# Optimization experiments

Measured on AMD Instinct MI355X. Metric: run time of the kernel, lower is better.

The kernel has to match this reference:

```python
import jax, jax.numpy as jnp
import numpy as np

EPS = 1e-6
D_CONV = 4

def _layernorm(x):
    m = jnp.mean(x, axis=-1, keepdims=True)
    v = jnp.mean((x - m) ** 2, axis=-1, keepdims=True)
    return (x - m) / jnp.sqrt(v + EPS)

def setup_inputs() -> dict:
    key = jax.random.key(0)
    ks = jax.random.split(key, 20)
    B, L, D = 2, 4096, 1024
    Di = D          # expand = 1
    N = 16          # d_state
    R = 64          # dt_rank = ceil(D/16)
    H = 4 * D       # mlp hidden
    s = 0.02
    rn = lambda k, sh: s * jax.random.normal(k, sh, dtype=jnp.float32)
    x = jax.random.normal(ks[0], (B, L, D), dtype=jnp.float32)
    path = jax.random.permutation(ks[1], L).astype(jnp.int32)
    path_rev = jnp.argsort(path).astype(jnp.int32)
    A_log = jnp.log(jnp.tile(jnp.arange(1, N + 1, dtype=jnp.float32)[None, :], (Di, 1)))
    return {
        'x': x, 'path': path, 'path_rev': path_rev,
        'in_proj_w': rn(ks[2], (2 * Di, D)),
        'conv_w': rn(ks[3], (Di, D_CONV)), 'conv_b': rn(ks[4], (Di,)),
        'x_proj_w': rn(ks[5], (R + 2 * N, Di)),
        'dt_proj_w': rn(ks[6], (Di, R)), 'dt_proj_b': rn(ks[7], (Di,)),
        'A_log': A_log, 'D_param': jnp.ones((Di,), dtype=jnp.float32),
        'out_proj_w': rn(ks[8], (D, Di)),
        'fc1_w': rn(ks[9], (H, D)), 'fc1_b': jnp.zeros((H,), dtype=jnp.float32),
        'fc2_w': rn(ks[10], (D, H)), 'fc2_b': jnp.zeros((D,), dtype=jnp.float32),
    }

def _mamba(u, in_proj_w, conv_w, conv_b, x_proj_w, dt_proj_w, dt_proj_b, A_log, D_param, out_proj_w):
    B, L, _ = u.shape
    N = A_log.shape[1]
    R = dt_proj_w.shape[1]
    xz = u @ in_proj_w.T                      # (B,L,2*Di)
    xi, z = jnp.split(xz, 2, axis=-1)
    # causal depthwise conv1d, kernel 4
    xpad = jnp.pad(xi, ((0, 0), (D_CONV - 1, 0), (0, 0)))
    xc = conv_b + sum(conv_w[:, k] * xpad[:, k:k + L, :] for k in range(D_CONV))
    xc = jax.nn.silu(xc)                      # (B,L,Di)
    proj = xc @ x_proj_w.T                    # (B,L,R+2N)
    dt_r = proj[..., :R]
    Bm = proj[..., R:R + N]                   # (B,L,N)
    Cm = proj[..., R + N:]                    # (B,L,N)
    dt = jax.nn.softplus(dt_r @ dt_proj_w.T + dt_proj_b)  # (B,L,Di)
    A = -jnp.exp(A_log)                       # (Di,N)

    def step(h, inp):
        dt_t, B_t, C_t, x_t = inp             # (B,Di),(B,N),(B,N),(B,Di)
        dA = jnp.exp(dt_t[:, :, None] * A)    # (B,Di,N)
        h = dA * h + (dt_t * x_t)[:, :, None] * B_t[:, None, :]
        y = jnp.einsum('bdn,bn->bd', h, C_t)
        return h, y

    h0 = jnp.zeros((B, xc.shape[-1], N), dtype=u.dtype)
    xs = (dt.transpose(1, 0, 2), Bm.transpose(1, 0, 2), Cm.transpose(1, 0, 2), xc.transpose(1, 0, 2))
    _, ys = jax.lax.scan(step, h0, xs)        # (L,B,Di)
    y = ys.transpose(1, 0, 2) + D_param * xc
    y = y * jax.nn.silu(z)
    return y @ out_proj_w.T

def reference(x, path, path_rev, in_proj_w, conv_w, conv_b, x_proj_w, dt_proj_w, dt_proj_b,
              A_log, D_param, out_proj_w, fc1_w, fc1_b, fc2_w, fc2_b):
    tmp1 = x[:, path, :]                      # zigzag gather
    tmp1 = _mamba(_layernorm(tmp1), in_proj_w, conv_w, conv_b, x_proj_w,
                  dt_proj_w, dt_proj_b, A_log, D_param, out_proj_w)
    x = x + tmp1[:, path_rev, :]              # zigzag scatter (inverse gather)
    h = _layernorm(x)
    h = jax.nn.gelu(h @ fc1_w.T + fc1_b, approximate=True) @ fc2_w.T + fc2_b
    return x + h
```

## Files before the change

kernel.cpp:

```cpp
#include <hip/hip_runtime.h>
#include <cstdint>
#include <cstddef>

typedef unsigned short u16;
typedef __bf16 bf16x8 __attribute__((ext_vector_type(8)));
typedef float f32x4 __attribute__((ext_vector_type(4)));
typedef u16 u16x8 __attribute__((ext_vector_type(8)));

#define B_ 2
#define L_ 4096
#define D_ 1024
#define N_ 16
#define BL_ 8192
#define NC_ 64
#define LC_ 64

__device__ __forceinline__ float bf2f(u16 h) {
  union { unsigned int u; float f; } v; v.u = ((unsigned int)h) << 16; return v.f;
}
__device__ __forceinline__ u16 f2bf(float f) {
  union { float f; unsigned int u; } v; v.f = f;
  unsigned int r = v.u + 0x7FFFu + ((v.u >> 16) & 1u);
  return (u16)(r >> 16);
}
__device__ __forceinline__ float sigmoidf_(float x) { return 1.0f / (1.0f + __expf(-x)); }

#define WBF_TOT 11730944
__global__ __launch_bounds__(256) void cvt_w_k(
    const float* __restrict__ s0, const float* __restrict__ s1,
    const float* __restrict__ s2, const float* __restrict__ s3,
    const float* __restrict__ s4, const float* __restrict__ s5,
    u16* __restrict__ dst)
{
  int i = blockIdx.x * 256 + threadIdx.x;
  if (i >= WBF_TOT) return;
  float v;
  if (i < 2097152) v = s0[i];
  else if (i < 2228224) { int j = i - 2097152; v = (j < 98304) ? s1[j] : 0.0f; }
  else if (i < 2293760) v = s2[i - 2228224];
  else if (i < 3342336) v = s3[i - 2293760];
  else if (i < 7536640) v = s4[i - 3342336];
  else v = s5[i - 7536640];
  dst[i] = f2bf(v);
}

#define BK 32
enum { M_BF16 = 0, M_PROJ = 1, M_SOFTPLUS = 2, M_GELU = 3, M_BIASRES = 4 };

#define GLDS(gp, lp) __builtin_amdgcn_global_load_lds( \
    (const __attribute__((address_space(1))) void*)(gp), \
    (__attribute__((address_space(3))) void*)(lp), 16, 0, 0)

template<int MODE>
__device__ __forceinline__ void epi_store(
    float v, size_t row, int col, int Nn,
    float* __restrict__ C, u16* __restrict__ C2,
    const float* __restrict__ bias, const u16* __restrict__ resid)
{
  if constexpr (MODE == M_BF16) {
    C2[row * Nn + col] = f2bf(v);
  } else if constexpr (MODE == M_PROJ) {
    C[row * 96 + col] = v;
    if (col < 64) C2[(row << 6) + col] = f2bf(v);
  } else if constexpr (MODE == M_SOFTPLUS) {
    v += bias[col];
    v = (v > 20.0f) ? v : log1pf(__expf(v));
    C2[row * Nn + col] = f2bf(v);
  } else if constexpr (MODE == M_GELU) {
    v += bias[col];
    float a = 0.7978845608028654f * (v + 0.044715f * v * v * v);
    float t = 1.0f - 2.0f / (__expf(2.0f * a) + 1.0f);
    C2[row * Nn + col] = f2bf(0.5f * v * (1.0f + t));
  } else if constexpr (MODE == M_BIASRES) {
    C[row * Nn + col] = v + bias[col] + bf2f(resid[row * Nn + col]);
  }
}

#define BM 128
#define BN 128

template<int MODE, int K>
__global__ __launch_bounds__(256, 2) void gemm_bt(
    const u16* __restrict__ A, const u16* __restrict__ W,
    float* __restrict__ C, u16* __restrict__ C2,
    const float* __restrict__ bias, const u16* __restrict__ resid,
    int M, int N)
{
  __shared__ __align__(16) u16 As[3][BM * BK];
  __shared__ __align__(16) u16 Bs[3][BN * BK];

  const int id = blockIdx.x + gridDim.x * blockIdx.y;
  const int xcd = id & 7;
  const int qq = id >> 3;
  const int bandH = gridDim.y >> 3;
  const int xs = qq % gridDim.x;
  const int ys = xcd * bandH + qq / gridDim.x;
  const int bm = ys * BM;
  const int bn = xs * BN;

  const int tid = threadIdx.x;
  const int lane = tid & 63;
  const int wave = tid >> 6;
  const int wr = (wave >> 1) * 64;
  const int wc = (wave & 1) * 64;

  f32x4 acc[4][4];
#pragma unroll
  for (int i = 0; i < 4; ++i)
#pragma unroll
    for (int j = 0; j < 4; ++j)
#pragma unroll
      for (int r = 0; r < 4; ++r) acc[i][j][r] = 0.0f;

  const int r0 = tid >> 2;
  const int ke = (((tid & 3) ^ (r0 & 3)) << 3);
  const u16* Ab = A + (size_t)(bm + r0) * K + ke;
  const u16* Wb = W + (size_t)(bn + r0) * K + ke;
  constexpr size_t rstep = (size_t)64 * K;

  auto issue = [&](int buf, int k0) {
    GLDS(Ab + k0, &As[buf][tid * 8]);
    GLDS(Ab + k0 + rstep, &As[buf][(tid + 256) * 8]);
    GLDS(Wb + k0, &Bs[buf][tid * 8]);
    GLDS(Wb + k0 + rstep, &Bs[buf][(tid + 256) * 8]);
  };

  issue(0, 0);
  if constexpr (BK < K) issue(1, BK);

  const int mr = lane & 15;
  const int pos = (((lane >> 4) ^ (mr & 3)) << 3);
  constexpr int NIT = K / BK;

  auto step = [&](int it) {
    if (it + 1 < NIT) asm volatile("s_waitcnt vmcnt(4)" ::: "memory");
    else              asm volatile("s_waitcnt vmcnt(0)" ::: "memory");
    asm volatile("s_barrier" ::: "memory");
    if (it + 2 < NIT) issue((it + 2) % 3, (it + 2) * BK);
    const int cur = it % 3;
    bf16x8 af[4], bfr[4];
#pragma unroll
    for (int i = 0; i < 4; ++i)
      af[i] = *(const bf16x8*)(&As[cur][(wr + i * 16 + mr) * BK + pos]);
#pragma unroll
    for (int j = 0; j < 4; ++j)
      bfr[j] = *(const bf16x8*)(&Bs[cur][(wc + j * 16 + mr) * BK + pos]);
#pragma unroll
    for (int i = 0; i < 4; ++i)
#pragma unroll
      for (int j = 0; j < 4; ++j)
        acc[i][j] = __builtin_amdgcn_mfma_f32_16x16x32_bf16(af[i], bfr[j], acc[i][j], 0, 0, 0);
  };

  if constexpr (NIT <= 32) {
#pragma unroll
    for (int it = 0; it < NIT; ++it) step(it);
  } else {
#pragma unroll 6
    for (int it = 0; it < NIT; ++it) step(it);
  }

  const int mlo = (lane >> 4) << 2;
  const int nlo = lane & 15;
#pragma unroll
  for (int i = 0; i < 4; ++i) {
#pragma unroll
    for (int j = 0; j < 4; ++j) {
      int col = bn + wc + j * 16 + nlo;
      if (col < N) {
#pragma unroll
        for (int r = 0; r < 4; ++r) {
          size_t row = (size_t)(bm + wr + i * 16 + mlo + r);
          epi_store<MODE>(acc[i][j][r], row, col, N, C, C2, bias, resid);
        }
      }
    }
  }
}

#define BM2 128
#define BN2 256

template<int MODE, int K>
__global__ __launch_bounds__(256, 2) void gemm_big(
    const u16* __restrict__ A, const u16* __restrict__ W,
    float* __restrict__ C, u16* __restrict__ C2,
    const float* __restrict__ bias, const u16* __restrict__ resid,
    int M, int N)
{
  __shared__ __align__(16) u16 As[3][BM2 * BK];
  __shared__ __align__(16) u16 Bs[3][BN2 * BK];

  const int id = blockIdx.x + gridDim.x * blockIdx.y;
  const int xcd = id & 7;
  const int qq = id >> 3;
  const int bandH = gridDim.y >> 3;
  const int xs = qq % gridDim.x;
  const int ys = xcd * bandH + qq / gridDim.x;
  const int bm = ys * BM2;
  const int bn = xs * BN2;

  const int tid = threadIdx.x;
  const int lane = tid & 63;
  const int wave = tid >> 6;
  const int wm = (wave >> 1) * 64;
  const int wn = (wave & 1) * 128;

  f32x4 acc[4][8];
#pragma unroll
  for (int i = 0; i < 4; ++i)
#pragma unroll
    for (int j = 0; j < 8; ++j)
#pragma unroll
      for (int r = 0; r < 4; ++r) acc[i][j][r] = 0.0f;

  const int r0 = tid >> 2;
  const int ke = (((tid & 3) ^ (r0 & 3)) << 3);
  const u16* Ab = A + (size_t)(bm + r0) * K + ke;
  const u16* Wb = W + (size_t)(bn + r0) * K + ke;
  constexpr size_t rstep = (size_t)64 * K;

  auto issue = [&](int buf, int k0) {
    GLDS(Ab + k0, &As[buf][tid * 8]);
    GLDS(Ab + k0 + rstep, &As[buf][(tid + 256) * 8]);
    GLDS(Wb + k0, &Bs[buf][tid * 8]);
    GLDS(Wb + k0 + rstep,     &Bs[buf][(tid + 256) * 8]);
    GLDS(Wb + k0 + 2 * rstep, &Bs[buf][(tid + 512) * 8]);
    GLDS(Wb + k0 + 3 * rstep, &Bs[buf][(tid + 768) * 8]);
  };

  issue(0, 0);
  issue(1, BK);

  const int mr = lane & 15;
  const int pos = (((lane >> 4) ^ (mr & 3)) << 3);
  constexpr int NIT = K / BK;

  auto step = [&](int it) {
    if (it + 1 < NIT) asm volatile("s_waitcnt vmcnt(6)" ::: "memory");
    else              asm volatile("s_waitcnt vmcnt(0)" ::: "memory");
    asm volatile("s_barrier" ::: "memory");
    if (it + 2 < NIT) issue((it + 2) % 3, (it + 2) * BK);
    const int cur = it % 3;
    bf16x8 af[4], bfr[8];
#pragma unroll
    for (int i = 0; i < 4; ++i)
      af[i] = *(const bf16x8*)(&As[cur][(wm + i * 16 + mr) * BK + pos]);
#pragma unroll
    for (int j = 0; j < 8; ++j)
      bfr[j] = *(const bf16x8*)(&Bs[cur][(wn + j * 16 + mr) * BK + pos]);
#pragma unroll
    for (int i = 0; i < 4; ++i)
#pragma unroll
      for (int j = 0; j < 8; ++j)
        acc[i][j] = __builtin_amdgcn_mfma_f32_16x16x32_bf16(af[i], bfr[j], acc[i][j], 0, 0, 0);
  };

  if constexpr (NIT <= 32) {
#pragma unroll
    for (int it = 0; it < NIT; ++it) step(it);
  } else {
#pragma unroll 6
    for (int it = 0; it < NIT; ++it) step(it);
  }

  const int mlo = (lane >> 4) << 2;
  const int nlo = lane & 15;
#pragma unroll
  for (int i = 0; i < 4; ++i) {
#pragma unroll
    for (int j = 0; j < 8; ++j) {
      int col = bn + wn + j * 16 + nlo;
#pragma unroll
      for (int r = 0; r < 4; ++r) {
        size_t row = (size_t)(bm + wm + i * 16 + mlo + r);
        epi_store<MODE>(acc[i][j][r], row, col, N, C, C2, bias, resid);
      }
    }
  }
}

__device__ __forceinline__ void blockReduce2(float& s, float& q) {
#pragma unroll
  for (int o = 32; o > 0; o >>= 1) { s += __shfl_down(s, o, 64); q += __shfl_down(q, o, 64); }
  __shared__ float red[2][4];
  int lane = threadIdx.x & 63, wave = threadIdx.x >> 6;
  if (lane == 0) { red[0][wave] = s; red[1][wave] = q; }
  __syncthreads();
  s = red[0][0] + red[0][1] + red[0][2] + red[0][3];
  q = red[1][0] + red[1][1] + red[1][2] + red[1][3];
}

__global__ __launch_bounds__(256) void ln_gather_k(
    const float* __restrict__ x, const int* __restrict__ path, u16* __restrict__ out)
{
  int b = blockIdx.x >> 12;
  int l = blockIdx.x & 4095;
  int src = path[l];
  const float* row = x + (((size_t)b * L_ + src) << 10);
  u16* orow = out + (((size_t)b * L_ + l) << 10);
  float v[4], s = 0.f, q = 0.f;
#pragma unroll
  for (int i = 0; i < 4; ++i) {
    v[i] = row[threadIdx.x + (i << 8)];
    s += v[i]; q += v[i] * v[i];
  }
  blockReduce2(s, q);
  float mean = s * (1.0f / 1024.0f);
  float var = q * (1.0f / 1024.0f) - mean * mean;
  float rstd = rsqrtf(var + 1e-6f);
#pragma unroll
  for (int i = 0; i < 4; ++i)
    orow[threadIdx.x + (i << 8)] = f2bf((v[i] - mean) * rstd);
}

__global__ __launch_bounds__(256) void ln_scatter_k(
    const float* __restrict__ x, const int* __restrict__ prev,
    const u16* __restrict__ mo, u16* __restrict__ xnew, u16* __restrict__ lnout)
{
  int b = blockIdx.x >> 12;
  int l = blockIdx.x & 4095;
  int pl = prev[l];
  const float* xr = x + (((size_t)b * L_ + l) << 10);
  const u16* mr_ = mo + (((size_t)b * L_ + pl) << 10);
  size_t base = ((size_t)blockIdx.x) << 10;
  float v[4], s = 0.f, q = 0.f;
#pragma unroll
  for (int i = 0; i < 4; ++i) {
    v[i] = xr[threadIdx.x + (i << 8)] + bf2f(mr_[threadIdx.x + (i << 8)]);
    s += v[i]; q += v[i] * v[i];
  }
  blockReduce2(s, q);
  float mean = s * (1.0f / 1024.0f);
  float var = q * (1.0f / 1024.0f) - mean * mean;
  float rstd = rsqrtf(var + 1e-6f);
#pragma unroll
  for (int i = 0; i < 4; ++i) {
    xnew[base + threadIdx.x + (i << 8)] = f2bf(v[i]);
    lnout[base + threadIdx.x + (i << 8)] = f2bf((v[i] - mean) * rstd);
  }
}

__global__ __launch_bounds__(256) void conv_silu_k(
    const u16* __restrict__ xz, const float* __restrict__ cw, const float* __restrict__ cb,
    u16* __restrict__ xc)
{
  int t = blockIdx.x * 256 + threadIdx.x;
  int d0 = (t & 127) << 3;
  int l  = (t >> 7) & 4095;
  int b  = t >> 19;
  float acc[8];
  f32x4 cb0 = *(const f32x4*)(&cb[d0]);
  f32x4 cb1 = *(const f32x4*)(&cb[d0 + 4]);
#pragma unroll
  for (int j = 0; j < 4; ++j) { acc[j] = cb0[j]; acc[4 + j] = cb1[j]; }
  f32x4 cwv[8];
#pragma unroll
  for (int j = 0; j < 8; ++j) cwv[j] = *(const f32x4*)(&cw[(d0 + j) << 2]);
#pragma unroll
  for (int k = 0; k < 4; ++k) {
    int ls = l + k - 3;
    if (ls >= 0) {
      u16x8 v = *(const u16x8*)(&xz[(((size_t)b * L_ + ls) << 11) + d0]);
#pragma unroll
      for (int j = 0; j < 8; ++j)
        acc[j] += cwv[j][k] * bf2f(v[j]);
    }
  }
  u16x8 o;
#pragma unroll
  for (int j = 0; j < 8; ++j) {
    float a = acc[j];
    a = a * sigmoidf_(a);
    o[j] = f2bf(a);
  }
  *(u16x8*)(&xc[(size_t)t << 3]) = o;
}

__global__ __launch_bounds__(256) void scan_p1_k(
    const u16* __restrict__ dt, const u16* __restrict__ xc, const float* __restrict__ proj,
    const float* __restrict__ A_log, float* __restrict__ acum, float* __restrict__ hloc)
{
  int c = blockIdx.x & (NC_ - 1);
  int q = (blockIdx.x >> 6) & 3;
  int b = blockIdx.x >> 8;
  int d = (q << 8) + threadIdx.x;
  float Arow[N_];
#pragma unroll
  for (int n = 0; n < N_; ++n) Arow[n] = -__expf(A_log[(d << 4) + n]);
  float h[N_], ac[N_];
#pragma unroll
  for (int n = 0; n < N_; ++n) { h[n] = 0.0f; ac[n] = 1.0f; }
  int l0 = c << 6;
  for (int i = 0; i < LC_; ++i) {
    size_t rowb = (size_t)b * L_ + (l0 + i);
    float dtv = bf2f(dt[(rowb << 10) + d]);
    float xv = bf2f(xc[(rowb << 10) + d]);
    float dtx = dtv * xv;
    const float* Bp = proj + rowb * 96 + 64;
#pragma unroll
    for (int n = 0; n < N_; ++n) {
      float dA = __expf(dtv * Arow[n]);
      h[n] = dA * h[n] + dtx * Bp[n];
      ac[n] *= dA;
    }
  }
  size_t sb = ((((size_t)b << 10) + d) << 10) + (c << 4);
#pragma unroll
  for (int n = 0; n < N_; ++n) { acum[sb + n] = ac[n]; hloc[sb + n] = h[n]; }
}

__global__ __launch_bounds__(256) void scan_p2_k(
    const float* __restrict__ acum, const float* __restrict__ hloc, float* __restrict__ hin)
{
  int idx = blockIdx.x * 256 + threadIdx.x;
  int n = idx & 15;
  int dn = idx >> 4;
  size_t base = ((size_t)dn << 10) + n;
  float hs = 0.0f;
  for (int c = 0; c < NC_; ++c) {
    hin[base + (c << 4)] = hs;
    hs = acum[base + (c << 4)] * hs + hloc[base + (c << 4)];
  }
}

__global__ __launch_bounds__(256) void scan_p3_k(
    const u16* __restrict__ dt, const u16* __restrict__ xc, const float* __restrict__ proj,
    const float* __restrict__ A_log, const float* __restrict__ Dp, const float* __restrict__ hin,
    const u16* __restrict__ xz, u16* __restrict__ yg)
{
  int c = blockIdx.x & (NC_ - 1);
  int q = (blockIdx.x >> 6) & 3;
  int b = blockIdx.x >> 8;
  int d = (q << 8) + threadIdx.x;
  float Arow[N_];
#pragma unroll
  for (int n = 0; n < N_; ++n) Arow[n] = -__expf(A_log[(d << 4) + n]);
  float h[N_];
  size_t sb = ((((size_t)b << 10) + d) << 10) + (c << 4);
#pragma unroll
  for (int n = 0; n < N_; ++n) h[n] = hin[sb + n];
  float Dv = Dp[d];
  int l0 = c << 6;
  for (int i = 0; i < LC_; ++i) {
    size_t rowb = (size_t)b * L_ + (l0 + i);
    float dtv = bf2f(dt[(rowb << 10) + d]);
    float xv = bf2f(xc[(rowb << 10) + d]);
    float dtx = dtv * xv;
    const float* Bp = proj + rowb * 96 + 64;
    const float* Cp = proj + rowb * 96 + 80;
    float y = 0.0f;
#pragma unroll
    for (int n = 0; n < N_; ++n) {
      float dA = __expf(dtv * Arow[n]);
      h[n] = dA * h[n] + dtx * Bp[n];
      y += h[n] * Cp[n];
    }
    y += Dv * xv;
    float zv = bf2f(xz[(rowb << 11) + 1024 + d]);
    yg[(rowb << 10) + d] = f2bf(y * zv * sigmoidf_(zv));
  }
}

extern "C" void kernel_launch(void* const* d_in, const int* in_sizes, int n_in,
                              void* d_out, int out_size, void* d_ws, size_t ws_size,
                              hipStream_t stream)
{
  const float* x_in      = (const float*)d_in[0];
  const int*   path      = (const int*)d_in[1];
  const int*   path_rev  = (const int*)d_in[2];
  const float* in_proj_w = (const float*)d_in[3];
  const float* conv_w    = (const float*)d_in[4];
  const float* conv_b    = (const float*)d_in[5];
  const float* x_proj_w  = (const float*)d_in[6];
  const float* dt_proj_w = (const float*)d_in[7];
  const float* dt_proj_b = (const float*)d_in[8];
  const float* A_log     = (const float*)d_in[9];
  const float* Dp        = (const float*)d_in[10];
  const float* out_pw    = (const float*)d_in[11];
  const float* fc1_w     = (const float*)d_in[12];
  const float* fc1_b     = (const float*)d_in[13];
  const float* fc2_w     = (const float*)d_in[14];
  const float* fc2_b     = (const float*)d_in[15];
  float* out = (float*)d_out;

  char* w = (char*)d_ws;
  size_t off = 0;
  auto alloc = [&](size_t bytes) -> char* {
    char* p = w + off;
    off = (off + bytes + 255) & ~(size_t)255;
    return p;
  };
  u16*   wbf   = (u16*)  alloc((size_t)WBF_TOT * 2);
  u16*   ln_bf = (u16*)  alloc((size_t)BL_ * 1024 * 2);
  u16*   xz    = (u16*)  alloc((size_t)BL_ * 2048 * 2);
  u16*   xc    = (u16*)  alloc((size_t)BL_ * 1024 * 2);
  char*  pool0 = alloc(0);
  float* proj  = (float*)alloc((size_t)BL_ * 96 * 4);
  u16*   dtr   = (u16*)  alloc((size_t)BL_ * 64 * 2);
  u16*   dt    = (u16*)  alloc((size_t)BL_ * 1024 * 2);
  float* acum  = (float*)alloc((size_t)2 * 1024 * NC_ * 16 * 4);
  float* hloc  = (float*)alloc((size_t)2 * 1024 * NC_ * 16 * 4);
  float* hin   = (float*)alloc((size_t)2 * 1024 * NC_ * 16 * 4);
  u16*   yg    = (u16*)  alloc((size_t)BL_ * 1024 * 2);
  u16*   h1b   = (u16*)pool0;
  off = (size_t)(pool0 - w) + ((size_t)BL_ * 4096 * 2);
  u16*   xnew  = (u16*)  alloc((size_t)BL_ * 1024 * 2);
  u16*   mo    = xz;

  const u16* w_inp = wbf;
  const u16* w_xp  = wbf + 2097152;
  const u16* w_dtp = wbf + 2228224;
  const u16* w_op  = wbf + 2293760;
  const u16* w_fc1 = wbf + 3342336;
  const u16* w_fc2 = wbf + 7536640;

  dim3 blk(256);
  cvt_w_k<<<WBF_TOT / 256, blk, 0, stream>>>(in_proj_w, x_proj_w, dt_proj_w, out_pw,
                                             fc1_w, fc2_w, wbf);
  ln_gather_k<<<BL_, blk, 0, stream>>>(x_in, path, ln_bf);
  gemm_big<M_BF16, 1024><<<dim3(8, 64), blk, 0, stream>>>(ln_bf, w_inp, nullptr, xz, nullptr, nullptr, 8192, 2048);
  conv_silu_k<<<(BL_ * 128) / 256, blk, 0, stream>>>(xz, conv_w, conv_b, xc);
  gemm_bt<M_PROJ, 1024><<<dim3(1, 64), blk, 0, stream>>>(xc, w_xp, proj, dtr, nullptr, nullptr, 8192, 96);
  gemm_bt<M_SOFTPLUS, 64><<<dim3(8, 64), blk, 0, stream>>>(dtr, w_dtp, nullptr, dt, dt_proj_b, nullptr, 8192, 1024);
  scan_p1_k<<<2 * 4 * NC_, blk, 0, stream>>>(dt, xc, proj, A_log, acum, hloc);
  scan_p2_k<<<(2 * 1024 * 16) / 256, blk, 0, stream>>>(acum, hloc, hin);
  scan_p3_k<<<2 * 4 * NC_, blk, 0, stream>>>(dt, xc, proj, A_log, Dp, hin, xz, yg);
  gemm_bt<M_BF16, 1024><<<dim3(8, 64), blk, 0, stream>>>(yg, w_op, nullptr, mo, nullptr, nullptr, 8192, 1024);
  ln_scatter_k<<<BL_, blk, 0, stream>>>(x_in, path_rev, mo, xnew, ln_bf);
  gemm_big<M_GELU, 1024><<<dim3(16, 64), blk, 0, stream>>>(ln_bf, w_fc1, nullptr, h1b, fc1_b, nullptr, 8192, 4096);
  gemm_bt<M_BIASRES, 4096><<<dim3(8, 64), blk, 0, stream>>>(h1b, w_fc2, out, nullptr, fc2_b, xnew, 8192, 1024);
}
```

Measured before the change: 583.0 us.

## Use 256x256 eight-phase pipelined GEMM and split-K fc2 with combine kernel

Replaces the 128x256 GEMM with a 512-thread kernel using 256x256 tiles and 64-wide K steps. It double-buffers LDS and interleaves LDS reads, global-to-LDS staging and MFMA work across eight phases, with s_setprio raised around the MFMA blocks. The in_proj and fc1 GEMMs move to this kernel. fc2 is also split along K into two fp32 partial buffers that reuse the dead ln_bf/xz/xc region, and a new elementwise kernel adds the partials, bias and residual. The larger tiles aim to raise operand reuse per LDS byte and hide memory latency. The cost is heavier register/LDS use and extra fp32 partial-sum traffic for fc2.

```diff
diff --git a/kernel.cpp b/kernel.cpp
--- a/kernel.cpp
+++ b/kernel.cpp
@@ -45,7 +45,7 @@
 }
 
 #define BK 32
-enum { M_BF16 = 0, M_PROJ = 1, M_SOFTPLUS = 2, M_GELU = 3, M_BIASRES = 4 };
+enum { M_BF16 = 0, M_PROJ = 1, M_SOFTPLUS = 2, M_GELU = 3, M_BIASRES = 4, M_F32 = 5 };
 
 #define GLDS(gp, lp) __builtin_amdgcn_global_load_lds( \
     (const __attribute__((address_space(1))) void*)(gp), \
@@ -73,6 +73,8 @@
     C2[row * Nn + col] = f2bf(0.5f * v * (1.0f + t));
   } else if constexpr (MODE == M_BIASRES) {
     C[row * Nn + col] = v + bias[col] + bf2f(resid[row * Nn + col]);
+  } else if constexpr (MODE == M_F32) {
+    C[row * Nn + col] = v;
   }
 }
 
@@ -178,18 +180,27 @@
   }
 }
 
-#define BM2 128
-#define BN2 256
-
-template<int MODE, int K>
-__global__ __launch_bounds__(256, 2) void gemm_big(
+#define P_MID asm volatile("s_barrier" ::: "memory")
+#define P_END asm volatile("s_barrier" ::: "memory")
+#define P_LG0 asm volatile("s_waitcnt lgkmcnt(0)" ::: "memory")
+#define P_VM2 asm volatile("s_waitcnt vmcnt(2)" ::: "memory")
+#define P_SB0 __builtin_amdgcn_sched_barrier(0)
+
+#define PH(RD1, RD2, STG, MH, NH, VMW) \
+  RD1; RD2; STG; \
+  P_MID; P_LG0; P_SB0; \
+  __builtin_amdgcn_s_setprio(1); mm(MH, NH); P_SB0; __builtin_amdgcn_s_setprio(0); \
+  VMW; P_END;
+
+template<int MODE, int KFULL, int KSPLIT>
+__global__ __launch_bounds__(512, 2) void gemm256(
     const u16* __restrict__ A, const u16* __restrict__ W,
     float* __restrict__ C, u16* __restrict__ C2,
     const float* __restrict__ bias, const u16* __restrict__ resid,
     int M, int N)
 {
-  __shared__ __align__(16) u16 As[3][BM2 * BK];
-  __shared__ __align__(16) u16 Bs[3][BN2 * BK];
+  __shared__ __align__(16) u16 As[2][16384];
+  __shared__ __align__(16) u16 Bs[2][16384];
 
   const int id = blockIdx.x + gridDim.x * blockIdx.y;
   const int xcd = id & 7;
@@ -197,87 +208,122 @@
   const int bandH = gridDim.y >> 3;
   const int xs = qq % gridDim.x;
   const int ys = xcd * bandH + qq / gridDim.x;
-  const int bm = ys * BM2;
-  const int bn = xs * BN2;
+  const int bm = ys * 256;
+  const int bn = xs * 256;
+  const int z = blockIdx.z;
 
   const int tid = threadIdx.x;
   const int lane = tid & 63;
   const int wave = tid >> 6;
-  const int wm = (wave >> 1) * 64;
-  const int wn = (wave & 1) * 128;
-
-  f32x4 acc[4][8];
-#pragma unroll
-  for (int i = 0; i < 4; ++i)
-#pragma unroll
-    for (int j = 0; j < 8; ++j)
+  const int wm = (wave >> 2) * 128;
+  const int wn = (wave & 3) * 64;
+  const int mr = lane & 15;
+  const int kq = lane >> 4;
+
+  f32x4 acc[8][4];
+#pragma unroll
+  for (int i = 0; i < 8; ++i)
+#pragma unroll
+    for (int j = 0; j < 4; ++j)
 #pragma unroll
       for (int r = 0; r < 4; ++r) acc[i][j][r] = 0.0f;
 
-  const int r0 = tid >> 2;
-  const int ke = (((tid & 3) ^ (r0 & 3)) << 3);
-  const u16* Ab = A + (size_t)(bm + r0) * K + ke;
-  const u16* Wb = W + (size_t)(bn + r0) * K + ke;
-  constexpr size_t rstep = (size_t)64 * K;
-
-  auto issue = [&](int buf, int k0) {
-    GLDS(Ab + k0, &As[buf][tid * 8]);
-    GLDS(Ab + k0 + rstep, &As[buf][(tid + 256) * 8]);
-    GLDS(Wb + k0, &Bs[buf][tid * 8]);
-    GLDS(Wb + k0 + rstep,     &Bs[buf][(tid + 256) * 8]);
-    GLDS(Wb + k0 + 2 * rstep, &Bs[buf][(tid + 512) * 8]);
-    GLDS(Wb + k0 + 3 * rstep, &Bs[buf][(tid + 768) * 8]);
-  };
-
-  issue(0, 0);
-  issue(1, BK);
-
-  const int mr = lane & 15;
-  const int pos = (((lane >> 4) ^ (mr & 3)) << 3);
-  constexpr int NIT = K / BK;
-
-  auto step = [&](int it) {
-    if (it + 1 < NIT) asm volatile("s_waitcnt vmcnt(6)" ::: "memory");
-    else              asm volatile("s_waitcnt vmcnt(0)" ::: "memory");
-    asm volatile("s_barrier" ::: "memory");
-    if (it + 2 < NIT) issue((it + 2) % 3, (it + 2) * BK);
-    const int cur = it % 3;
-    bf16x8 af[4], bfr[8];
-#pragma unroll
-    for (int i = 0; i < 4; ++i)
-      af[i] = *(const bf16x8*)(&As[cur][(wm + i * 16 + mr) * BK + pos]);
-#pragma unroll
-    for (int j = 0; j < 8; ++j)
-      bfr[j] = *(const bf16x8*)(&Bs[cur][(wn + j * 16 + mr) * BK + pos]);
-#pragma unroll
-    for (int i = 0; i < 4; ++i)
-#pragma unroll
-      for (int j = 0; j < 8; ++j)
-        acc[i][j] = __builtin_amdgcn_mfma_f32_16x16x32_bf16(af[i], bfr[j], acc[i][j], 0, 0, 0);
-  };
-
-  if constexpr (NIT <= 32) {
-#pragma unroll
-    for (int it = 0; it < NIT; ++it) step(it);
-  } else {
-#pragma unroll 6
-    for (int it = 0; it < NIT; ++it) step(it);
-  }
+  const int row0 = tid >> 3;
+  const int g = (tid & 7) ^ (row0 & 7);
+  const u16* Asrc = A + (size_t)(bm + row0) * KFULL + (size_t)z * KSPLIT + g * 8;
+  const u16* Wsrc = W + (size_t)(bn + row0) * KFULL + (size_t)z * KSPLIT + g * 8;
+
+  auto stage = [&](int buf, int which , int T) {
+    const int h = which & 1;
+    const u16* s = ((which < 2) ? Asrc : Wsrc) + (size_t)(h * 128) * KFULL + T * 64;
+    u16* d = (which < 2) ? &As[buf][h * 8192] : &Bs[buf][h * 8192];
+    GLDS(s, d + tid * 8);
+    GLDS(s + (size_t)64 * KFULL, d + (tid + 512) * 8);
+  };
+
+  bf16x8 Ar[8], Br[4];
+  const int sl0 = ((kq ^ (mr & 7)) << 3);
+  const int aB = (wm + mr) * 64;
+  const int bB = (wn + mr) * 64;
+
+  auto dsA = [&](int buf, int mh) {
+#pragma unroll
+    for (int i2 = 0; i2 < 4; ++i2) {
+      Ar[i2 * 2 + 0] = *(const bf16x8*)&As[buf][aB + (mh * 4 + i2) * 1024 + sl0];
+      Ar[i2 * 2 + 1] = *(const bf16x8*)&As[buf][aB + (mh * 4 + i2) * 1024 + (sl0 ^ 32)];
+    }
+  };
+  auto dsB = [&](int buf, int nh) {
+#pragma unroll
+    for (int j2 = 0; j2 < 2; ++j2) {
+      Br[j2 * 2 + 0] = *(const bf16x8*)&Bs[buf][bB + (nh * 2 + j2) * 1024 + sl0];
+      Br[j2 * 2 + 1] = *(const bf16x8*)&Bs[buf][bB + (nh * 2 + j2) * 1024 + (sl0 ^ 32)];
+    }
+  };
+  auto mm = [&](int mh, int nh) {
+#pragma unroll
+    for (int i2 = 0; i2 < 4; ++i2)
+#pragma unroll
+      for (int j2 = 0; j2 < 2; ++j2) {
+        acc[mh * 4 + i2][nh * 2 + j2] = __builtin_amdgcn_mfma_f32_16x16x32_bf16(
+            Ar[i2 * 2 + 0], Br[j2 * 2 + 0], acc[mh * 4 + i2][nh * 2 + j2], 0, 0, 0);
+        acc[mh * 4 + i2][nh * 2 + j2] = __builtin_amdgcn_mfma_f32_16x16x32_bf16(
+            Ar[i2 * 2 + 1], Br[j2 * 2 + 1], acc[mh * 4 + i2][nh * 2 + j2], 0, 0, 0);
+      }
+  };
+
+  stage(0, 0, 0); stage(0, 1, 0); stage(0, 2, 0); stage(0, 3, 0);
+  stage(1, 0, 1);
+  P_VM2;
+  asm volatile("s_barrier" ::: "memory");
+
+  constexpr int NT = KSPLIT / 64;
+  constexpr int NT2 = NT / 2;
+#pragma unroll 1
+  for (int t = 0; t < NT2; ++t) {
+    const int T1 = 2 * t + 1, T2p = 2 * t + 2, T3 = 2 * t + 3;
+    PH(dsA(0, 0), dsB(0, 0), stage(1, 1, T1), 0, 0, );
+    PH(dsB(0, 1),          , stage(1, 2, T1), 0, 1, );
+    PH(dsA(0, 1),          , stage(1, 3, T1), 1, 1, );
+    PH(dsB(0, 0),          , stage(0, 0, T2p), 1, 0, P_VM2);
+    PH(dsA(1, 0), dsB(1, 0), stage(0, 1, T2p), 0, 0, );
+    PH(dsB(1, 1),          , stage(0, 2, T2p), 0, 1, );
+    PH(dsA(1, 1),          , stage(0, 3, T2p), 1, 1, );
+    PH(dsB(1, 0),          , stage(1, 0, T3), 1, 0, P_VM2);
+  }
+  asm volatile("s_waitcnt vmcnt(0)" ::: "memory");
 
   const int mlo = (lane >> 4) << 2;
   const int nlo = lane & 15;
-#pragma unroll
-  for (int i = 0; i < 4; ++i) {
-#pragma unroll
-    for (int j = 0; j < 8; ++j) {
+  float* Cz = C;
+  if constexpr (MODE == M_F32) Cz = C + (size_t)z * ((size_t)M * (size_t)N);
+#pragma unroll
+  for (int i = 0; i < 8; ++i)
+#pragma unroll
+    for (int j = 0; j < 4; ++j) {
       int col = bn + wn + j * 16 + nlo;
 #pragma unroll
       for (int r = 0; r < 4; ++r) {
         size_t row = (size_t)(bm + wm + i * 16 + mlo + r);
-        epi_store<MODE>(acc[i][j][r], row, col, N, C, C2, bias, resid);
+        epi_store<MODE>(acc[i][j][r], row, col, N, Cz, C2, bias, resid);
       }
     }
-  }
+}
+
+__global__ __launch_bounds__(256) void fc2_comb_k(
+    const float* __restrict__ p, const float* __restrict__ bias,
+    const u16* __restrict__ resid, float* __restrict__ out)
+{
+  size_t i = ((((size_t)blockIdx.x << 8) + threadIdx.x) << 2);
+  f32x4 a = *(const f32x4*)(p + i);
+  f32x4 b = *(const f32x4*)(p + 8388608 + i);
+  int col = (int)(i & 1023);
+  f32x4 bs = *(const f32x4*)(bias + col);
+  const u16* rr = resid + i;
+  f32x4 o;
+#pragma unroll
+  for (int j = 0; j < 4; ++j) o[j] = a[j] + b[j] + bs[j] + bf2f(rr[j]);
+  *(f32x4*)(out + i) = o;
 }
 
 __device__ __forceinline__ void blockReduce2(float& s, float& q) {
@@ -507,6 +553,7 @@
   off = (size_t)(pool0 - w) + ((size_t)BL_ * 4096 * 2);
   u16*   xnew  = (u16*)  alloc((size_t)BL_ * 1024 * 2);
   u16*   mo    = xz;
+  float* pf    = (float*)ln_bf;
 
   const u16* w_inp = wbf;
   const u16* w_xp  = wbf + 2097152;
@@ -516,10 +563,11 @@
   const u16* w_fc2 = wbf + 7536640;
 
   dim3 blk(256);
+  dim3 blk5(512);
   cvt_w_k<<<WBF_TOT / 256, blk, 0, stream>>>(in_proj_w, x_proj_w, dt_proj_w, out_pw,
                                              fc1_w, fc2_w, wbf);
   ln_gather_k<<<BL_, blk, 0, stream>>>(x_in, path, ln_bf);
-  gemm_big<M_BF16, 1024><<<dim3(8, 64), blk, 0, stream>>>(ln_bf, w_inp, nullptr, xz, nullptr, nullptr, 8192, 2048);
+  gemm256<M_BF16, 1024, 1024><<<dim3(8, 32, 1), blk5, 0, stream>>>(ln_bf, w_inp, nullptr, xz, nullptr, nullptr, 8192, 2048);
   conv_silu_k<<<(BL_ * 128) / 256, blk, 0, stream>>>(xz, conv_w, conv_b, xc);
   gemm_bt<M_PROJ, 1024><<<dim3(1, 64), blk, 0, stream>>>(xc, w_xp, proj, dtr, nullptr, nullptr, 8192, 96);
   gemm_bt<M_SOFTPLUS, 64><<<dim3(8, 64), blk, 0, stream>>>(dtr, w_dtp, nullptr, dt, dt_proj_b, nullptr, 8192, 1024);
@@ -528,6 +576,7 @@
   scan_p3_k<<<2 * 4 * NC_, blk, 0, stream>>>(dt, xc, proj, A_log, Dp, hin, xz, yg);
   gemm_bt<M_BF16, 1024><<<dim3(8, 64), blk, 0, stream>>>(yg, w_op, nullptr, mo, nullptr, nullptr, 8192, 1024);
   ln_scatter_k<<<BL_, blk, 0, stream>>>(x_in, path_rev, mo, xnew, ln_bf);
-  gemm_big<M_GELU, 1024><<<dim3(16, 64), blk, 0, stream>>>(ln_bf, w_fc1, nullptr, h1b, fc1_b, nullptr, 8192, 4096);
-  gemm_bt<M_BIASRES, 4096><<<dim3(8, 64), blk, 0, stream>>>(h1b, w_fc2, out, nullptr, fc2_b, xnew, 8192, 1024);
-}
+  gemm256<M_GELU, 1024, 1024><<<dim3(16, 32, 1), blk5, 0, stream>>>(ln_bf, w_fc1, nullptr, h1b, fc1_b, nullptr, 8192, 4096);
+  gemm256<M_F32, 4096, 2048><<<dim3(4, 32, 2), blk5, 0, stream>>>(h1b, w_fc2, pf, nullptr, nullptr, nullptr, 8192, 1024);
+  fc2_comb_k<<<8192, blk, 0, stream>>>(pf, fc2_b, xnew, out);
+}
```

After: 579.6 us. About the same (-0.6%).

## Drop 128x256 GEMM, use 128x128 tiles with higher occupancy and setprio

Applied to the files above, without the earlier changes.

Removes the 128x256 gemm_big kernel and routes in_proj and fc1 through the 128x128 gemm_bt kernel with twice as many blocks. Raises gemm_bt launch bounds to 3 blocks per CU. Changes the LDS XOR swizzle to key on row>>1 instead of row, aiming to cut bank conflicts. Raises wave priority with s_setprio around the MFMA block. Smaller tiles lower arithmetic intensity per block and add global traffic. The tighter register budget from the higher launch bound may cause spills.

```diff
diff --git a/kernel.cpp b/kernel.cpp
--- a/kernel.cpp
+++ b/kernel.cpp
@@ -80,7 +80,7 @@
 #define BN 128
 
 template<int MODE, int K>
-__global__ __launch_bounds__(256, 2) void gemm_bt(
+__global__ __launch_bounds__(256, 3) void gemm_bt(
     const u16* __restrict__ A, const u16* __restrict__ W,
     float* __restrict__ C, u16* __restrict__ C2,
     const float* __restrict__ bias, const u16* __restrict__ resid,
@@ -113,7 +113,7 @@
       for (int r = 0; r < 4; ++r) acc[i][j][r] = 0.0f;
 
   const int r0 = tid >> 2;
-  const int ke = (((tid & 3) ^ (r0 & 3)) << 3);
+  const int ke = (((tid & 3) ^ ((r0 >> 1) & 3)) << 3);
   const u16* Ab = A + (size_t)(bm + r0) * K + ke;
   const u16* Wb = W + (size_t)(bn + r0) * K + ke;
   constexpr size_t rstep = (size_t)64 * K;
@@ -129,7 +129,7 @@
   if constexpr (BK < K) issue(1, BK);
 
   const int mr = lane & 15;
-  const int pos = (((lane >> 4) ^ (mr & 3)) << 3);
+  const int pos = (((lane >> 4) ^ ((mr >> 1) & 3)) << 3);
   constexpr int NIT = K / BK;
 
   auto step = [&](int it) {
@@ -145,11 +145,13 @@
 #pragma unroll
     for (int j = 0; j < 4; ++j)
       bfr[j] = *(const bf16x8*)(&Bs[cur][(wc + j * 16 + mr) * BK + pos]);
+    __builtin_amdgcn_s_setprio(1);
 #pragma unroll
     for (int i = 0; i < 4; ++i)
 #pragma unroll
       for (int j = 0; j < 4; ++j)
         acc[i][j] = __builtin_amdgcn_mfma_f32_16x16x32_bf16(af[i], bfr[j], acc[i][j], 0, 0, 0);
+    __builtin_amdgcn_s_setprio(0);
   };
 
   if constexpr (NIT <= 32) {
@@ -173,108 +175,6 @@
           size_t row = (size_t)(bm + wr + i * 16 + mlo + r);
           epi_store<MODE>(acc[i][j][r], row, col, N, C, C2, bias, resid);
         }
-      }
-    }
-  }
-}
-
-#define BM2 128
-#define BN2 256
-
-template<int MODE, int K>
-__global__ __launch_bounds__(256, 2) void gemm_big(
-    const u16* __restrict__ A, const u16* __restrict__ W,
-    float* __restrict__ C, u16* __restrict__ C2,
-    const float* __restrict__ bias, const u16* __restrict__ resid,
-    int M, int N)
-{
-  __shared__ __align__(16) u16 As[3][BM2 * BK];
-  __shared__ __align__(16) u16 Bs[3][BN2 * BK];
-
-  const int id = blockIdx.x + gridDim.x * blockIdx.y;
-  const int xcd = id & 7;
-  const int qq = id >> 3;
-  const int bandH = gridDim.y >> 3;
-  const int xs = qq % gridDim.x;
-  const int ys = xcd * bandH + qq / gridDim.x;
-  const int bm = ys * BM2;
-  const int bn = xs * BN2;
-
-  const int tid = threadIdx.x;
-  const int lane = tid & 63;
-  const int wave = tid >> 6;
-  const int wm = (wave >> 1) * 64;
-  const int wn = (wave & 1) * 128;
-
-  f32x4 acc[4][8];
-#pragma unroll
-  for (int i = 0; i < 4; ++i)
-#pragma unroll
-    for (int j = 0; j < 8; ++j)
-#pragma unroll
-      for (int r = 0; r < 4; ++r) acc[i][j][r] = 0.0f;
-
-  const int r0 = tid >> 2;
-  const int ke = (((tid & 3) ^ (r0 & 3)) << 3);
-  const u16* Ab = A + (size_t)(bm + r0) * K + ke;
-  const u16* Wb = W + (size_t)(bn + r0) * K + ke;
-  constexpr size_t rstep = (size_t)64 * K;
-
-  auto issue = [&](int buf, int k0) {
-    GLDS(Ab + k0, &As[buf][tid * 8]);
-    GLDS(Ab + k0 + rstep, &As[buf][(tid + 256) * 8]);
-    GLDS(Wb + k0, &Bs[buf][tid * 8]);
-    GLDS(Wb + k0 + rstep,     &Bs[buf][(tid + 256) * 8]);
-    GLDS(Wb + k0 + 2 * rstep, &Bs[buf][(tid + 512) * 8]);
-    GLDS(Wb + k0 + 3 * rstep, &Bs[buf][(tid + 768) * 8]);
-  };
-
-  issue(0, 0);
-  issue(1, BK);
-
-  const int mr = lane & 15;
-  const int pos = (((lane >> 4) ^ (mr & 3)) << 3);
-  constexpr int NIT = K / BK;
-
-  auto step = [&](int it) {
-    if (it + 1 < NIT) asm volatile("s_waitcnt vmcnt(6)" ::: "memory");
-    else              asm volatile("s_waitcnt vmcnt(0)" ::: "memory");
-    asm volatile("s_barrier" ::: "memory");
-    if (it + 2 < NIT) issue((it + 2) % 3, (it + 2) * BK);
-    const int cur = it % 3;
-    bf16x8 af[4], bfr[8];
-#pragma unroll
-    for (int i = 0; i < 4; ++i)
-      af[i] = *(const bf16x8*)(&As[cur][(wm + i * 16 + mr) * BK + pos]);
-#pragma unroll
-    for (int j = 0; j < 8; ++j)
-      bfr[j] = *(const bf16x8*)(&Bs[cur][(wn + j * 16 + mr) * BK + pos]);
-#pragma unroll
-    for (int i = 0; i < 4; ++i)
-#pragma unroll
-      for (int j = 0; j < 8; ++j)
-        acc[i][j] = __builtin_amdgcn_mfma_f32_16x16x32_bf16(af[i], bfr[j], acc[i][j], 0, 0, 0);
-  };
-
-  if constexpr (NIT <= 32) {
-#pragma unroll
-    for (int it = 0; it < NIT; ++it) step(it);
-  } else {
-#pragma unroll 6
-    for (int it = 0; it < NIT; ++it) step(it);
-  }
-
-  const int mlo = (lane >> 4) << 2;
-  const int nlo = lane & 15;
-#pragma unroll
-  for (int i = 0; i < 4; ++i) {
-#pragma unroll
-    for (int j = 0; j < 8; ++j) {
-      int col = bn + wn + j * 16 + nlo;
-#pragma unroll
-      for (int r = 0; r < 4; ++r) {
-        size_t row = (size_t)(bm + wm + i * 16 + mlo + r);
-        epi_store<MODE>(acc[i][j][r], row, col, N, C, C2, bias, resid);
       }
     }
   }
@@ -519,7 +419,7 @@
   cvt_w_k<<<WBF_TOT / 256, blk, 0, stream>>>(in_proj_w, x_proj_w, dt_proj_w, out_pw,
                                              fc1_w, fc2_w, wbf);
   ln_gather_k<<<BL_, blk, 0, stream>>>(x_in, path, ln_bf);
-  gemm_big<M_BF16, 1024><<<dim3(8, 64), blk, 0, stream>>>(ln_bf, w_inp, nullptr, xz, nullptr, nullptr, 8192, 2048);
+  gemm_bt<M_BF16, 1024><<<dim3(16, 64), blk, 0, stream>>>(ln_bf, w_inp, nullptr, xz, nullptr, nullptr, 8192, 2048);
   conv_silu_k<<<(BL_ * 128) / 256, blk, 0, stream>>>(xz, conv_w, conv_b, xc);
   gemm_bt<M_PROJ, 1024><<<dim3(1, 64), blk, 0, stream>>>(xc, w_xp, proj, dtr, nullptr, nullptr, 8192, 96);
   gemm_bt<M_SOFTPLUS, 64><<<dim3(8, 64), blk, 0, stream>>>(dtr, w_dtp, nullptr, dt, dt_proj_b, nullptr, 8192, 1024);
@@ -528,6 +428,6 @@
   scan_p3_k<<<2 * 4 * NC_, blk, 0, stream>>>(dt, xc, proj, A_log, Dp, hin, xz, yg);
   gemm_bt<M_BF16, 1024><<<dim3(8, 64), blk, 0, stream>>>(yg, w_op, nullptr, mo, nullptr, nullptr, 8192, 1024);
   ln_scatter_k<<<BL_, blk, 0, stream>>>(x_in, path_rev, mo, xnew, ln_bf);
-  gemm_big<M_GELU, 1024><<<dim3(16, 64), blk, 0, stream>>>(ln_bf, w_fc1, nullptr, h1b, fc1_b, nullptr, 8192, 4096);
+  gemm_bt<M_GELU, 1024><<<dim3(32, 64), blk, 0, stream>>>(ln_bf, w_fc1, nullptr, h1b, fc1_b, nullptr, 8192, 4096);
   gemm_bt<M_BIASRES, 4096><<<dim3(8, 64), blk, 0, stream>>>(h1b, w_fc2, out, nullptr, fc2_b, xnew, 8192, 1024);
 }
```

Result: no change. 585.5 us (+0.4%).
